# Kernel optimization log

Measured on AMD Instinct MI355X. Metric: run time of the kernel, lower is better.

Reference implementation:

```python
import jax, jax.numpy as jnp
import numpy as np

N, Q, C, T = 32, 300, 92, 32  # batch, queries, classes, targets-per-image
L_CLS, L_IOU, L_L1 = 1.0, 2.0, 5.0


def _cxcywh_to_xyxy(b):
    cx, cy, w, h = b[..., 0], b[..., 1], b[..., 2], b[..., 3]
    return jnp.stack([cx - 0.5 * w, cy - 0.5 * h, cx + 0.5 * w, cy + 0.5 * h], axis=-1)


def _generalized_box_iou(a, b):
    # a: [P,4] xyxy, b: [M,4] xyxy -> [P,M]
    area_a = (a[:, 2] - a[:, 0]) * (a[:, 3] - a[:, 1])
    area_b = (b[:, 2] - b[:, 0]) * (b[:, 3] - b[:, 1])
    lt = jnp.maximum(a[:, None, :2], b[None, :, :2])
    rb = jnp.minimum(a[:, None, 2:], b[None, :, 2:])
    wh = jnp.clip(rb - lt, 0.0)
    inter = wh[..., 0] * wh[..., 1]
    union = area_a[:, None] + area_b[None, :] - inter
    iou = inter / union
    lt_c = jnp.minimum(a[:, None, :2], b[None, :, :2])
    rb_c = jnp.maximum(a[:, None, 2:], b[None, :, 2:])
    wh_c = jnp.clip(rb_c - lt_c, 0.0)
    area_c = wh_c[..., 0] * wh_c[..., 1]
    return iou - (area_c - union) / area_c


def _cost_matrix(pred_logits, pred_boxes, tgt_labels, tgt_boxes):
    out_prob = jax.nn.softmax(pred_logits.reshape(-1, C), axis=-1)  # [N*Q, C]
    out_bbox = pred_boxes.reshape(-1, 4)                            # [N*Q, 4]
    cost_class = -out_prob[:, tgt_labels]                           # [N*Q, N*T]
    cost_bbox = jnp.sum(jnp.abs(out_bbox[:, None, :] - tgt_boxes[None, :, :]), axis=-1)
    cost_giou = -_generalized_box_iou(_cxcywh_to_xyxy(out_bbox), _cxcywh_to_xyxy(tgt_boxes))
    cost = L_L1 * cost_bbox + L_CLS * cost_class + L_IOU * cost_giou
    return cost.reshape(N, Q, N * T)


def _lsa(cost):
    # Jonker-Volgenant shortest augmenting path (e-maxx), cost: [n, m], n <= m.
    # Returns col4row: for each row, the assigned column.
    n, m = cost.shape
    INF = np.inf
    u = np.zeros(n + 1)
    v = np.zeros(m + 1)
    p = np.zeros(m + 1, dtype=np.int64)   # p[j] = row assigned to column j (1-based)
    way = np.zeros(m + 1, dtype=np.int64)
    for i in range(1, n + 1):
        p[0] = i
        j0 = 0
        minv = np.full(m + 1, INF)
        used = np.zeros(m + 1, dtype=bool)
        while True:
            used[j0] = True
            i0 = p[j0]
            free = ~used[1:]
            cur = cost[i0 - 1] - u[i0] - v[1:]
            upd = free & (cur < minv[1:])
            minv[1:][upd] = cur[upd]
            way[1:][upd] = j0
            j1 = 1 + int(np.argmin(np.where(free, minv[1:], INF)))
            delta = minv[j1]
            used_idx = np.nonzero(used)[0]
            u[p[used_idx]] += delta
            v[used_idx] -= delta
            minv[1:][free] -= delta
            j0 = j1
            if p[j0] == 0:
                break
        while j0:
            j1 = way[j0]
            p[j0] = p[j1]
            j0 = j1
    ans = np.full(n, -1, dtype=np.int64)
    js = np.nonzero(p[1:])[0]
    ans[p[1:][js] - 1] = js
    return ans


def _multiplier(cost):
    c_np = np.asarray(jax.device_get(cost))  # [N, Q, N*T]
    mult = np.zeros_like(c_np)
    for i in range(N):
        block = c_np[i, :, i * T:(i + 1) * T]  # [Q, T], sample i's own targets
        q_of_t = _lsa(block.T)                 # for each target, matched query
        # NOTE: faithfully replicates the original code's `count = 0` reset,
        # so columns are indexed locally (first T columns of the global axis).
        mult[i, q_of_t, np.arange(T)] = 1.0
    return jnp.asarray(mult)


def setup_inputs() -> dict:
    key = jax.random.key(0)
    k1, k2, k3, k4 = jax.random.split(key, 4)
    return {
        "pred_logits": jax.random.normal(k1, (N, Q, C), dtype=jnp.float32),
        "pred_boxes": jax.random.uniform(k2, (N, Q, 4), dtype=jnp.float32),
        "tgt_labels": jax.random.randint(k3, (N * T,), 0, C, dtype=jnp.int64),
        "tgt_boxes": jax.random.uniform(k4, (N * T, 4), dtype=jnp.float32),
    }


def reference(pred_logits, pred_boxes, tgt_labels, tgt_boxes):
    cost = _cost_matrix(pred_logits, pred_boxes, tgt_labels, tgt_boxes)
    mult = _multiplier(cost)
    return jnp.sum(cost * mult)
```

## Files before the change

kernel.cpp:

```cpp
#include <hip/hip_runtime.h>
#include <cfloat>
#include <cmath>

#define Nn 32
#define Qq 300
#define Cc 92
#define Tt 32
#define KCOLS 5
#define LSTRIDE 93
#define AUCTION_ROUNDS 6

__device__ inline float wave_min_bcast(float x) {
#define DPPMIN(ctrl) { int _t = __builtin_amdgcn_update_dpp( \
        __float_as_int(x), __float_as_int(x), ctrl, 0xf, 0xf, false); \
        x = fminf(x, __int_as_float(_t)); }
    DPPMIN(0x111) DPPMIN(0x112) DPPMIN(0x114) DPPMIN(0x118)
    DPPMIN(0x142) DPPMIN(0x143)
#undef DPPMIN
    return __int_as_float(__builtin_amdgcn_readlane(__float_as_int(x), 63));
}

__device__ inline int sel5i(const int a[KCOLS], int k) {
    int r = a[0];
    if (k == 1) r = a[1];
    if (k == 2) r = a[2];
    if (k == 3) r = a[3];
    if (k == 4) r = a[4];
    return r;
}

__device__ inline float readlane_f(float v, int lane) {
    return __int_as_float(__builtin_amdgcn_readlane(__float_as_int(v), lane));
}

__device__ inline void softmax_lds(const float* __restrict__ srow,
                                   float& mx, float& inv_s) {
    float m0 = -FLT_MAX, m1 = -FLT_MAX, m2 = -FLT_MAX, m3 = -FLT_MAX;
#pragma unroll
    for (int c = 0; c < Cc; c += 4) {
        m0 = fmaxf(m0, srow[c + 0]);
        m1 = fmaxf(m1, srow[c + 1]);
        m2 = fmaxf(m2, srow[c + 2]);
        m3 = fmaxf(m3, srow[c + 3]);
    }
    const float m = fmaxf(fmaxf(m0, m1), fmaxf(m2, m3));
    float s0 = 0.f, s1 = 0.f, s2 = 0.f, s3 = 0.f;
#pragma unroll
    for (int c = 0; c < Cc; c += 4) {
        s0 += __expf(srow[c + 0] - m);
        s1 += __expf(srow[c + 1] - m);
        s2 += __expf(srow[c + 2] - m);
        s3 += __expf(srow[c + 3] - m);
    }
    mx = m; inv_s = 1.f / ((s0 + s1) + (s2 + s3));
}

__device__ inline float det_cost(float cx, float cy, float w, float h,
                                 float bcx, float bcy, float bw, float bh,
                                 float cls) {
    const float ax0 = cx - 0.5f * w, ay0 = cy - 0.5f * h;
    const float ax1 = cx + 0.5f * w, ay1 = cy + 0.5f * h;
    const float areaA = (ax1 - ax0) * (ay1 - ay0);

    const float l1 = fabsf(cx - bcx) + fabsf(cy - bcy) +
                     fabsf(w - bw) + fabsf(h - bh);

    const float bx0 = bcx - 0.5f * bw, by0 = bcy - 0.5f * bh;
    const float bx1 = bcx + 0.5f * bw, by1 = bcy + 0.5f * bh;
    const float areaB = (bx1 - bx0) * (by1 - by0);

    const float ltx = fmaxf(ax0, bx0), lty = fmaxf(ay0, by0);
    const float rbx = fminf(ax1, bx1), rby = fminf(ay1, by1);
    const float iw = fmaxf(rbx - ltx, 0.f), ih = fmaxf(rby - lty, 0.f);
    const float inter = iw * ih;
    const float uni = areaA + areaB - inter;
    const float iou = inter / uni;

    const float ex0 = fminf(ax0, bx0), ey0 = fminf(ay0, by0);
    const float ex1 = fmaxf(ax1, bx1), ey1 = fmaxf(ay1, by1);
    const float areaC = fmaxf(ex1 - ex0, 0.f) * fmaxf(ey1 - ey0, 0.f);
    const float giou = iou - (areaC - uni) / areaC;

    return 5.f * l1 + cls - 2.f * giou;
}

__global__ __launch_bounds__(320) void fused_kernel(
    const float* __restrict__ logits,
    const float* __restrict__ pboxes,
    const int*   __restrict__ tlabels,
    const float* __restrict__ tboxes,
    float* __restrict__ out)
{
    const int b = blockIdx.x;
    const int tid = threadIdx.x;

    extern __shared__ float s_lg[];
    __shared__ float s_diag[Tt * Qq];
    __shared__ float s_tb[Tt * 4];
    __shared__ int   s_tl[Tt];
    __shared__ int   pairs[Tt];
    __shared__ float s_v[Qq];
    __shared__ float s_u[Tt + 1];
    __shared__ int   s_colrow[Qq];
    __shared__ unsigned s_bid[Qq];
    __shared__ int   s_bidrow[Qq];
    __shared__ unsigned s_mask;

    if (tid < Tt * 4) s_tb[tid] = tboxes[b * Tt * 4 + tid];
    if (tid < Tt)     s_tl[tid] = tlabels[b * Tt + tid];
    if (tid < Qq)     { s_v[tid] = 0.f; s_colrow[tid] = 0; }
    if (tid == 0)     s_mask = 0xffffffffu;

    {
        const float4* lgb = reinterpret_cast<const float4*>(
            logits + (size_t)b * Qq * Cc);
#pragma unroll 4
        for (int g = tid; g < Qq * 23; g += 320) {
            const float4 v = lgb[g];
            const int r = g / 23, c4 = (g - r * 23) * 4;
            float* dst = &s_lg[r * LSTRIDE + c4];
            dst[0] = v.x; dst[1] = v.y; dst[2] = v.z; dst[3] = v.w;
        }
    }
    __syncthreads();

    if (tid < Qq) {
        const float* srow = &s_lg[tid * LSTRIDE];
        float mx, inv_s;
        softmax_lds(srow, mx, inv_s);
        const float4 pbv = reinterpret_cast<const float4*>(pboxes)[b * Qq + tid];
#pragma unroll 4
        for (int t = 0; t < Tt; ++t) {
            const float cls = -__expf(srow[s_tl[t]] - mx) * inv_s;
            s_diag[t * Qq + tid] =
                det_cost(pbv.x, pbv.y, pbv.z, pbv.w,
                         s_tb[t * 4 + 0], s_tb[t * 4 + 1],
                         s_tb[t * 4 + 2], s_tb[t * 4 + 3], cls);
        }
    }
    __syncthreads();

    {
        const int w = tid >> 6, ln = tid & 63;
        const bool iv4 = (ln + 256) >= Qq;
        for (int round = 0; round < AUCTION_ROUNDS; ++round) {
            const unsigned msk = s_mask;
            if (msk == 0 || __popc(msk) <= 2) break;
            if (tid < Qq) { s_bid[tid] = 0u; s_bidrow[tid] = 0xffff; }
            __syncthreads();

            int row = 0;
            { unsigned m = msk; int cnt = w;
              while (m && cnt) { m &= m - 1; --cnt; }
              if (m) row = __ffs(m); }

            float g1 = 0.f, g2 = 0.f; int j1 = 0; unsigned mybid = 0;
            if (row) {
                const float* rowp = &s_diag[(row - 1) * Qq + ln];
                float m1 = INFINITY, m2 = INFINITY; int a1 = 0;
                float c;
                c = rowp[0]   - s_v[ln];
                if (c < m1) { m2 = m1; m1 = c; a1 = ln + 1; }   else if (c < m2) m2 = c;
                c = rowp[64]  - s_v[ln + 64];
                if (c < m1) { m2 = m1; m1 = c; a1 = ln + 65; }  else if (c < m2) m2 = c;
                c = rowp[128] - s_v[ln + 128];
                if (c < m1) { m2 = m1; m1 = c; a1 = ln + 129; } else if (c < m2) m2 = c;
                c = rowp[192] - s_v[ln + 192];
                if (c < m1) { m2 = m1; m1 = c; a1 = ln + 193; } else if (c < m2) m2 = c;
                c = iv4 ? INFINITY : (rowp[256] - s_v[ln + 256]);
                if (c < m1) { m2 = m1; m1 = c; a1 = ln + 257; } else if (c < m2) m2 = c;

                g1 = wave_min_bcast(m1);
                const unsigned long long mk = __ballot(m1 == g1);
                const int src = __ffsll((long long)mk) - 1;
                const float cand2 = (ln == src) ? m2 : m1;
                g2 = wave_min_bcast(cand2);
                j1 = __builtin_amdgcn_readlane(a1, src);
                mybid = __float_as_uint(g2 - g1) + 1u;
                if (ln == 0) atomicMax(&s_bid[j1 - 1], mybid);
            }
            __syncthreads();
            if (row && ln == 0 && s_bid[j1 - 1] == mybid)
                atomicMin(&s_bidrow[j1 - 1], row);
            __syncthreads();
            if (row && ln == 0) {
                if (s_bid[j1 - 1] == mybid && s_bidrow[j1 - 1] == row) {
                    const int old = s_colrow[j1 - 1];
                    s_colrow[j1 - 1] = row;
                    s_v[j1 - 1] -= (g2 - g1);
                    s_u[row] = g2;
                    atomicAnd(&s_mask, ~(1u << (row - 1)));
                    if (old) atomicOr(&s_mask, 1u << (old - 1));
                } else {
                    s_u[row] = g1;
                }
            }
            __syncthreads();
        }
    }

    if (tid >= 64) return;
    const int lane = tid;
    const bool inval4 = (lane + 256) >= Qq;

    float u_reg = (lane >= 1 && lane <= Tt) ? s_u[lane] : 0.f;
    float v_r[KCOLS]; int p_r[KCOLS];
#pragma unroll
    for (int k = 0; k < KCOLS; ++k) {
        const int j = lane + 64 * k;
        v_r[k] = (j < Qq) ? s_v[j] : 0.f;
        p_r[k] = (j < Qq) ? s_colrow[j] : 0;
    }

    for (unsigned rem = s_mask; rem; rem &= rem - 1) {
        const int i = __ffs(rem);

        float minv_r[KCOLS], vmask[KCOLS], am[KCOLS];
        int way_r[KCOLS];
#pragma unroll
        for (int k = 0; k < KCOLS; ++k) {
            minv_r[k] = FLT_MAX; way_r[k] = 0;
            const bool inv = (k == 4) && inval4;
            vmask[k] = inv ? -INFINITY : v_r[k];
            am[k]    = inv ?  INFINITY : 0.f;
        }
        float markg = 0.f;
        int   ent = 0;
        int   j0 = 0, i0 = i;
        float du = 0.f - readlane_f(u_reg, i);
        int   jfinal = 0;
        float Dfinal = 0.f;

        const float* rowp = &s_diag[(i0 - 1) * Qq + lane];
        float c0 = rowp[0], c1 = rowp[64], c2 = rowp[128], c3 = rowp[192],
              c4 = rowp[256];

        while (true) {
            const float cc[KCOLS] = {c0, c1, c2, c3, c4};
            float sv[KCOLS];
#pragma unroll
            for (int k = 0; k < KCOLS; ++k) {
                const float cur = (cc[k] + du) - vmask[k];
                const bool lt = cur < minv_r[k];
                way_r[k]  = lt ? j0  : way_r[k];
                minv_r[k] = lt ? cur : minv_r[k];
                sv[k] = minv_r[k] + am[k];
            }
            float val = sv[0];
            int   kb  = 0;
#pragma unroll
            for (int k = 1; k < KCOLS; ++k)
                if (sv[k] < val) { val = sv[k]; kb = k; }

            const float gmin = wave_min_bcast(val);
            const unsigned long long mask = __ballot(val == gmin);
            const int src = __ffsll((long long)mask) - 1;
            const int colid = lane + 1 + (kb << 6);
            const int pk = (sel5i(p_r, kb) << 16) | colid;
            const int got = __builtin_amdgcn_readlane(pk, src);
            const int j1   = got & 0xffff;
            const int rowm = got >> 16;

            const int k1 = (j1 - 1) >> 6;
            const bool own = (lane == ((j1 - 1) & 63));
#pragma unroll
            for (int k = 0; k < KCOLS; ++k)
                if (own && k == k1) { vmask[k] = -INFINITY; am[k] = INFINITY; }

            if (rowm == 0) { jfinal = j1; Dfinal = gmin; break; }

            i0 = rowm; j0 = j1;
            rowp = &s_diag[(i0 - 1) * Qq + lane];
            c0 = rowp[0]; c1 = rowp[64]; c2 = rowp[128]; c3 = rowp[192];
            c4 = rowp[256];
            du = gmin - readlane_f(u_reg, i0);
            markg = (lane == rowm) ? gmin : markg;
            ent   = (lane == rowm) ? 1    : ent;
        }

#pragma unroll
        for (int k = 0; k < KCOLS; ++k) {
            bool usedk = (am[k] == INFINITY);
            if (k == 4) usedk = usedk && !inval4;
            v_r[k] -= usedk ? (Dfinal - minv_r[k]) : 0.f;
        }
        u_reg += (lane == i) ? Dfinal : (ent ? (Dfinal - markg) : 0.f);

        int jj = jfinal;
        while (jj) {
            const int ow = (jj - 1) & 63, kk = (jj - 1) >> 6;
            const int jprev = __builtin_amdgcn_readlane(sel5i(way_r, kk), ow);
            int pnew;
            if (jprev == 0) pnew = i;
            else pnew = __builtin_amdgcn_readlane(sel5i(p_r, (jprev - 1) >> 6),
                                                  (jprev - 1) & 63);
            const bool own = (lane == ow);
#pragma unroll
            for (int k = 0; k < KCOLS; ++k) if (own && k == kk) p_r[k] = pnew;
            jj = jprev;
        }
    }

#pragma unroll
    for (int k = 0; k < KCOLS; ++k)
        if (p_r[k]) pairs[p_r[k] - 1] = lane + 64 * k;
    __threadfence_block();

    float part = 0.f;
    if (lane < Tt) {
        const int q = pairs[lane];
        const float* srow = &s_lg[q * LSTRIDE];
        float mx, inv_s;
        softmax_lds(srow, mx, inv_s);
        const float4 pbv = reinterpret_cast<const float4*>(pboxes)[b * Qq + q];
        const float4 tbv = reinterpret_cast<const float4*>(tboxes)[lane];
        const float cls = -__expf(srow[tlabels[lane]] - mx) * inv_s;
        part = det_cost(pbv.x, pbv.y, pbv.z, pbv.w,
                        tbv.x, tbv.y, tbv.z, tbv.w, cls);
    }
    for (int off = 32; off > 0; off >>= 1) part += __shfl_down(part, off);
    if (lane == 0) atomicAdd(out, part);
}

extern "C" void kernel_launch(void* const* d_in, const int* in_sizes, int n_in,
                              void* d_out, int out_size, void* d_ws, size_t ws_size,
                              hipStream_t stream) {
    const float* logits  = (const float*)d_in[0];
    const float* pboxes  = (const float*)d_in[1];
    const int*   tlabels = (const int*)d_in[2];
    const float* tboxes  = (const float*)d_in[3];
    float* out = (float*)d_out;

    (void)hipMemsetAsync(out, 0, sizeof(float), stream);
    const size_t lg_bytes = (size_t)Qq * LSTRIDE * sizeof(float);
    fused_kernel<<<Nn, 320, lg_bytes, stream>>>(logits, pboxes, tlabels, tboxes, out);
}
```

Before: 88.33 us.

## Bid on all unassigned rows per auction round with packed 64-bit bids

Each auction round now processes every unassigned row, spreading rows round-robin over the five waves, where before it handled at most one row per wave. Bid value and row id are packed into one 64-bit atomicMax, so a round needs one fewer barrier. The winner check moves to a per-row thread that reads stored bid data. The round cap goes from 6 to 16 and the early exit at two or fewer unassigned rows is removed. The aim is to assign more rows in the parallel auction and leave less work for the serial single-wave augmenting-path phase, at the cost of more auction rounds.

```diff
diff --git a/kernel.cpp b/kernel.cpp
--- a/kernel.cpp
+++ b/kernel.cpp
@@ -8,7 +8,7 @@
 #define Tt 32
 #define KCOLS 5
 #define LSTRIDE 93
-#define AUCTION_ROUNDS 6
+#define AUCTION_ROUNDS 16
 
 __device__ inline float wave_min_bcast(float x) {
 #define DPPMIN(ctrl) { int _t = __builtin_amdgcn_update_dpp( \
@@ -102,8 +102,9 @@
     __shared__ float s_v[Qq];
     __shared__ float s_u[Tt + 1];
     __shared__ int   s_colrow[Qq];
-    __shared__ unsigned s_bid[Qq];
-    __shared__ int   s_bidrow[Qq];
+    __shared__ unsigned long long s_bid64[Qq];
+    __shared__ int   s_rj1[Tt + 1];
+    __shared__ float s_rg1[Tt + 1], s_rg2[Tt + 1];
     __shared__ unsigned s_mask;
 
     if (tid < Tt * 4) s_tb[tid] = tboxes[b * Tt * 4 + tid];
@@ -145,51 +146,62 @@
         const bool iv4 = (ln + 256) >= Qq;
         for (int round = 0; round < AUCTION_ROUNDS; ++round) {
             const unsigned msk = s_mask;
-            if (msk == 0 || __popc(msk) <= 2) break;
-            if (tid < Qq) { s_bid[tid] = 0u; s_bidrow[tid] = 0xffff; }
+            if (msk == 0) break;
+            for (int j = tid; j < Qq; j += 320) s_bid64[j] = 0ull;
             __syncthreads();
 
-            int row = 0;
-            { unsigned m = msk; int cnt = w;
-              while (m && cnt) { m &= m - 1; --cnt; }
-              if (m) row = __ffs(m); }
-
-            float g1 = 0.f, g2 = 0.f; int j1 = 0; unsigned mybid = 0;
-            if (row) {
-                const float* rowp = &s_diag[(row - 1) * Qq + ln];
-                float m1 = INFINITY, m2 = INFINITY; int a1 = 0;
-                float c;
-                c = rowp[0]   - s_v[ln];
-                if (c < m1) { m2 = m1; m1 = c; a1 = ln + 1; }   else if (c < m2) m2 = c;
-                c = rowp[64]  - s_v[ln + 64];
-                if (c < m1) { m2 = m1; m1 = c; a1 = ln + 65; }  else if (c < m2) m2 = c;
-                c = rowp[128] - s_v[ln + 128];
-                if (c < m1) { m2 = m1; m1 = c; a1 = ln + 129; } else if (c < m2) m2 = c;
-                c = rowp[192] - s_v[ln + 192];
-                if (c < m1) { m2 = m1; m1 = c; a1 = ln + 193; } else if (c < m2) m2 = c;
-                c = iv4 ? INFINITY : (rowp[256] - s_v[ln + 256]);
-                if (c < m1) { m2 = m1; m1 = c; a1 = ln + 257; } else if (c < m2) m2 = c;
-
-                g1 = wave_min_bcast(m1);
-                const unsigned long long mk = __ballot(m1 == g1);
-                const int src = __ffsll((long long)mk) - 1;
-                const float cand2 = (ln == src) ? m2 : m1;
-                g2 = wave_min_bcast(cand2);
-                j1 = __builtin_amdgcn_readlane(a1, src);
-                mybid = __float_as_uint(g2 - g1) + 1u;
-                if (ln == 0) atomicMax(&s_bid[j1 - 1], mybid);
+            {
+                unsigned m = msk; int n = 0;
+                while (m) {
+                    const int row = __ffs(m);
+                    m &= m - 1;
+                    if ((n % 5) == w) {
+                        const float* rowp = &s_diag[(row - 1) * Qq + ln];
+                        float m1 = INFINITY, m2 = INFINITY; int a1 = 0;
+                        float c;
+                        c = rowp[0]   - s_v[ln];
+                        if (c < m1) { m2 = m1; m1 = c; a1 = ln + 1; }   else if (c < m2) m2 = c;
+                        c = rowp[64]  - s_v[ln + 64];
+                        if (c < m1) { m2 = m1; m1 = c; a1 = ln + 65; }  else if (c < m2) m2 = c;
+                        c = rowp[128] - s_v[ln + 128];
+                        if (c < m1) { m2 = m1; m1 = c; a1 = ln + 129; } else if (c < m2) m2 = c;
+                        c = rowp[192] - s_v[ln + 192];
+                        if (c < m1) { m2 = m1; m1 = c; a1 = ln + 193; } else if (c < m2) m2 = c;
+                        c = iv4 ? INFINITY : (rowp[256] - s_v[ln + 256]);
+                        if (c < m1) { m2 = m1; m1 = c; a1 = ln + 257; } else if (c < m2) m2 = c;
+
+                        const float g1 = wave_min_bcast(m1);
+                        const unsigned long long mk = __ballot(m1 == g1);
+                        const int src = __ffsll((long long)mk) - 1;
+                        const float cand2 = (ln == src) ? m2 : m1;
+                        const float g2 = wave_min_bcast(cand2);
+                        const int j1 = __builtin_amdgcn_readlane(a1, src);
+                        if (ln == 0) {
+                            s_rj1[row] = j1; s_rg1[row] = g1; s_rg2[row] = g2;
+                            const unsigned long long pk =
+                                ((unsigned long long)(__float_as_uint(g2 - g1) + 1u) << 32)
+                                | (unsigned)(0xffffffffu - (unsigned)row);
+                            atomicMax(&s_bid64[j1 - 1], pk);
+                        }
+                    }
+                    ++n;
+                }
             }
             __syncthreads();
-            if (row && ln == 0 && s_bid[j1 - 1] == mybid)
-                atomicMin(&s_bidrow[j1 - 1], row);
-            __syncthreads();
-            if (row && ln == 0) {
-                if (s_bid[j1 - 1] == mybid && s_bidrow[j1 - 1] == row) {
+
+            if (tid < Tt && (msk & (1u << tid))) {
+                const int row = tid + 1;
+                const int j1 = s_rj1[row];
+                const float g1 = s_rg1[row], g2 = s_rg2[row];
+                const unsigned long long mypk =
+                    ((unsigned long long)(__float_as_uint(g2 - g1) + 1u) << 32)
+                    | (unsigned)(0xffffffffu - (unsigned)row);
+                if (s_bid64[j1 - 1] == mypk) {
                     const int old = s_colrow[j1 - 1];
                     s_colrow[j1 - 1] = row;
                     s_v[j1 - 1] -= (g2 - g1);
                     s_u[row] = g2;
-                    atomicAnd(&s_mask, ~(1u << (row - 1)));
+                    atomicAnd(&s_mask, ~(1u << tid));
                     if (old) atomicOr(&s_mask, 1u << (old - 1));
                 } else {
                     s_u[row] = g1;
```

After: 83.55 us. -5.4%, faster.
